# Performance work log

Hardware: AMD Instinct MI355X
Metric: run time of the kernel (lower is better)

Reference implementation:

```python
import jax, jax.numpy as jnp
import numpy as np


def setup_inputs() -> dict:
    key = jax.random.key(0)
    x = jax.random.normal(key, (4096, 16384), dtype=jnp.float32)
    return {"x": x, "k": 128}


def reference(x, k):
    # top-k along last dim, ReLU the values, scatter back into zeros
    values, indices = jax.lax.top_k(x, k)            # [N, k]
    values = jax.nn.relu(values)
    rows = jnp.arange(x.shape[0])[:, None]            # [N, 1] broadcast over k
    result = jnp.zeros_like(x).at[rows, indices].set(values)
    return result
```

## Files before the change

### kernel.cpp

```cpp
#include <hip/hip_runtime.h>

#define T 1024
#define EPT 16
#define ROWLEN 16384
#define NW (T / 64)
#define B1 4096
#define B2 1024
#define CAP 768

__device__ __forceinline__ unsigned f2ord(float f) {
    unsigned b = __float_as_uint(f);
    return b ^ ((b & 0x80000000u) ? 0xFFFFFFFFu : 0x80000000u);
}
__device__ __forceinline__ float ord2f(unsigned u) {
    unsigned b = (u & 0x80000000u) ? (u ^ 0x80000000u) : ~u;
    return __uint_as_float(b);
}

__device__ __forceinline__ void select_bin(const int* hist, int BINS, int k,
                                           int* waveSum, int* sh_b, int* sh_k) {
    const int tid  = threadIdx.x;
    const int lane = tid & 63;
    const int w    = tid >> 6;

    int bpt = (BINS + T - 1) / T;
    int lo  = tid * bpt; if (lo > BINS) lo = BINS;
    int hi  = lo + bpt;  if (hi > BINS) hi = BINS;

    int p = 0;
    for (int d = lo; d < hi; ++d) p += hist[d];

    int v = p;
    #pragma unroll
    for (int off = 1; off < 64; off <<= 1) {
        int t2 = __shfl_down(v, off);
        if (lane + off < 64) v += t2;
    }
    if (lane == 0) waveSum[w] = v;
    __syncthreads();

    int carry = 0;
    #pragma unroll
    for (int w2 = 0; w2 < NW; ++w2) if (w2 > w) carry += waveSum[w2];

    int P  = v + carry;
    int Pn = P - p;
    if (P >= k && Pn < k) {
        int running = Pn;
        for (int d = hi - 1; d >= lo; --d) {
            running += hist[d];
            if (running >= k) {
                *sh_b = d;
                *sh_k = k - (running - hist[d]);
                break;
            }
        }
    }
    __syncthreads();
}

__global__ __launch_bounds__(T, 4) void topk_relu_scatter(
        const float* __restrict__ x, const int* __restrict__ kptr,
        float* __restrict__ out) {
    __shared__ int hist[B1];
    __shared__ int waveSum[NW];
    __shared__ int sh_b, sh_k;
    __shared__ int candCnt, sh_meq, sh_cnt;
    __shared__ unsigned candU[CAP];

    const int tid = threadIdx.x;
    const int row = blockIdx.x;
    const float4* xrow = (const float4*)(x + (size_t)row * ROWLEN);
    float4*       orow = (float4*)(out + (size_t)row * ROWLEN);

    unsigned u[EPT];
    #pragma unroll
    for (int j4 = 0; j4 < EPT / 4; ++j4) {
        float4 v = xrow[tid + T * j4];
        u[4 * j4 + 0] = f2ord(v.x);
        u[4 * j4 + 1] = f2ord(v.y);
        u[4 * j4 + 2] = f2ord(v.z);
        u[4 * j4 + 3] = f2ord(v.w);
    }

    int k = *kptr;

    #pragma unroll
    for (int i = 0; i < B1 / T; ++i) hist[tid + T * i] = 0;
    if (tid == 0) candCnt = 0;
    __syncthreads();
    #pragma unroll
    for (int j = 0; j < EPT; ++j) atomicAdd(&hist[u[j] >> 20], 1);
    __syncthreads();
    select_bin(hist, B1, k, waveSum, &sh_b, &sh_k);
    const unsigned b1 = (unsigned)sh_b; k = sh_k;

    #pragma unroll
    for (int j = 0; j < EPT; ++j) {
        if ((u[j] >> 20) == b1) {
            int p = atomicAdd(&candCnt, 1);
            if (p < CAP) candU[p] = u[j];
        }
    }
    __syncthreads();
    const int m = candCnt;

    unsigned ustar; int t_eq;
    if (m <= CAP) {
        #pragma unroll
        for (int i = 0; i < B2 / T; ++i) hist[tid + T * i] = 0;
        __syncthreads();
        if (tid < m) atomicAdd(&hist[(candU[tid] >> 10) & 0x3FFu], 1);
        __syncthreads();
        select_bin(hist, B2, k, waveSum, &sh_b, &sh_k);
        const unsigned pref22 = (b1 << 10) | (unsigned)sh_b; k = sh_k;

        for (int i = 0; i < B2 / T; ++i) hist[tid + T * i] = 0;
        __syncthreads();
        if (tid < m) {
            unsigned c = candU[tid];
            if ((c >> 10) == pref22) atomicAdd(&hist[c & 0x3FFu], 1);
        }
        __syncthreads();
        select_bin(hist, B2, k, waveSum, &sh_b, &sh_k);
        ustar = (pref22 << 10) | (unsigned)sh_b;
        t_eq  = sh_k;
    } else {
        #pragma unroll
        for (int i = 0; i < B1 / T; ++i) hist[tid + T * i] = 0;
        __syncthreads();
        #pragma unroll
        for (int j = 0; j < EPT; ++j)
            if ((u[j] >> 20) == b1) atomicAdd(&hist[(u[j] >> 8) & 0xFFFu], 1);
        __syncthreads();
        select_bin(hist, B1, k, waveSum, &sh_b, &sh_k);
        const unsigned pref24 = (b1 << 12) | (unsigned)sh_b; k = sh_k;

        for (int i = tid; i < 256; i += T) hist[i] = 0;
        __syncthreads();
        #pragma unroll
        for (int j = 0; j < EPT; ++j)
            if ((u[j] >> 8) == pref24) atomicAdd(&hist[u[j] & 0xFFu], 1);
        __syncthreads();
        select_bin(hist, 256, k, waveSum, &sh_b, &sh_k);
        ustar = (pref24 << 8) | (unsigned)sh_b;
        t_eq  = sh_k;
    }

    if (tid == 0) sh_meq = 0;
    __syncthreads();
    int local = 0;
    #pragma unroll
    for (int j = 0; j < EPT; ++j) local += (u[j] == ustar);
    if (local) atomicAdd(&sh_meq, local);
    __syncthreads();
    const int meq = sh_meq;

    int idxcut;
    if (t_eq >= meq) {
        idxcut = ROWLEN;
    } else {
        int lo = 0, hi = ROWLEN - 1;
        while (lo < hi) {
            int mid = (lo + hi) >> 1;
            if (tid == 0) sh_cnt = 0;
            __syncthreads();
            int c2 = 0;
            #pragma unroll
            for (int j = 0; j < EPT; ++j) {
                int idx = 4 * (tid + T * (j >> 2)) + (j & 3);
                c2 += (u[j] == ustar && idx <= mid);
            }
            if (c2) atomicAdd(&sh_cnt, c2);
            __syncthreads();
            int cnt = sh_cnt;
            __syncthreads();
            if (cnt >= t_eq) hi = mid; else lo = mid + 1;
        }
        idxcut = lo;
    }

    #pragma unroll
    for (int j4 = 0; j4 < EPT / 4; ++j4) {
        float4 o;
        float* op = &o.x;
        #pragma unroll
        for (int c = 0; c < 4; ++c) {
            unsigned uu = u[4 * j4 + c];
            int idx = 4 * (tid + T * j4) + c;
            bool sel = (uu > ustar) || (uu == ustar && idx <= idxcut);
            float xv = ord2f(uu);
            op[c] = (sel && xv > 0.0f) ? xv : 0.0f;
        }
        orow[tid + T * j4] = o;
    }
}

extern "C" void kernel_launch(void* const* d_in, const int* in_sizes, int n_in,
                              void* d_out, int out_size, void* d_ws, size_t ws_size,
                              hipStream_t stream) {
    const float* x    = (const float*)d_in[0];
    const int*   kptr = (const int*)d_in[1];
    float*       out  = (float*)d_out;
    int rows = in_sizes[0] / ROWLEN;
    topk_relu_scatter<<<rows, T, 0, stream>>>(x, kptr, out);
}
```

Before: 477.6 us.

## Rework top-k: positive-only histogram, streaming reload, candidate rank-sort with indices

Shrinks the block to 256 threads and stops holding the row in registers, re-reading it from global memory (mostly cache hits) in each pass. The first histogram counts only positive values. Output is written in one streaming pass with nontemporal stores, and boundary-bin candidates are collected together with their indices. The cut is then resolved by an O(m^2) shared-memory rank count that scatters only the selected candidates, replacing the two extra radix passes and the tie binary search. This removes register pressure and extra synchronisation phases in exchange for more global reloads and a quadratic candidate step.

```diff
diff --git a/kernel.cpp b/kernel.cpp
--- a/kernel.cpp
+++ b/kernel.cpp
@@ -1,12 +1,13 @@
 #include <hip/hip_runtime.h>
 
-#define T 1024
-#define EPT 16
+#define T 256
+#define NW (T / 64)
 #define ROWLEN 16384
-#define NW (T / 64)
+#define EPT4 (ROWLEN / T / 4)
 #define B1 4096
-#define B2 1024
-#define CAP 768
+#define CAP 1024
+
+typedef float __attribute__((ext_vector_type(4))) f32x4;
 
 __device__ __forceinline__ unsigned f2ord(float f) {
     unsigned b = __float_as_uint(f);
@@ -59,140 +60,168 @@
     __syncthreads();
 }
 
-__global__ __launch_bounds__(T, 4) void topk_relu_scatter(
+__global__ __launch_bounds__(T, 8) void topk_relu_scatter(
         const float* __restrict__ x, const int* __restrict__ kptr,
         float* __restrict__ out) {
     __shared__ int hist[B1];
     __shared__ int waveSum[NW];
-    __shared__ int sh_b, sh_k;
-    __shared__ int candCnt, sh_meq, sh_cnt;
-    __shared__ unsigned candU[CAP];
+    __shared__ int sh_b, sh_k, candCnt, sh_npos, sh_tmp;
+    unsigned* candU = (unsigned*)&hist[2048];
+    int*      candI = &hist[3072];
 
     const int tid = threadIdx.x;
     const int row = blockIdx.x;
     const float4* xrow = (const float4*)(x + (size_t)row * ROWLEN);
     float4*       orow = (float4*)(out + (size_t)row * ROWLEN);
 
-    unsigned u[EPT];
-    #pragma unroll
-    for (int j4 = 0; j4 < EPT / 4; ++j4) {
+    const int k = *kptr;
+
+    #pragma unroll
+    for (int i = 0; i < B1 / T; ++i) hist[tid + T * i] = 0;
+    if (tid == 0) { candCnt = 0; sh_npos = 0; }
+    __syncthreads();
+
+    int npos = 0;
+    #pragma unroll
+    for (int j4 = 0; j4 < EPT4; ++j4) {
         float4 v = xrow[tid + T * j4];
-        u[4 * j4 + 0] = f2ord(v.x);
-        u[4 * j4 + 1] = f2ord(v.y);
-        u[4 * j4 + 2] = f2ord(v.z);
-        u[4 * j4 + 3] = f2ord(v.w);
-    }
-
-    int k = *kptr;
-
-    #pragma unroll
-    for (int i = 0; i < B1 / T; ++i) hist[tid + T * i] = 0;
-    if (tid == 0) candCnt = 0;
-    __syncthreads();
-    #pragma unroll
-    for (int j = 0; j < EPT; ++j) atomicAdd(&hist[u[j] >> 20], 1);
-    __syncthreads();
-    select_bin(hist, B1, k, waveSum, &sh_b, &sh_k);
-    const unsigned b1 = (unsigned)sh_b; k = sh_k;
-
-    #pragma unroll
-    for (int j = 0; j < EPT; ++j) {
-        if ((u[j] >> 20) == b1) {
-            int p = atomicAdd(&candCnt, 1);
-            if (p < CAP) candU[p] = u[j];
-        }
-    }
-    __syncthreads();
-    const int m = candCnt;
-
-    unsigned ustar; int t_eq;
-    if (m <= CAP) {
         #pragma unroll
-        for (int i = 0; i < B2 / T; ++i) hist[tid + T * i] = 0;
-        __syncthreads();
-        if (tid < m) atomicAdd(&hist[(candU[tid] >> 10) & 0x3FFu], 1);
-        __syncthreads();
-        select_bin(hist, B2, k, waveSum, &sh_b, &sh_k);
-        const unsigned pref22 = (b1 << 10) | (unsigned)sh_b; k = sh_k;
-
-        for (int i = 0; i < B2 / T; ++i) hist[tid + T * i] = 0;
-        __syncthreads();
-        if (tid < m) {
-            unsigned c = candU[tid];
-            if ((c >> 10) == pref22) atomicAdd(&hist[c & 0x3FFu], 1);
-        }
-        __syncthreads();
-        select_bin(hist, B2, k, waveSum, &sh_b, &sh_k);
-        ustar = (pref22 << 10) | (unsigned)sh_b;
-        t_eq  = sh_k;
+        for (int c = 0; c < 4; ++c) {
+            unsigned u = f2ord((&v.x)[c]);
+            if (u & 0x80000000u) {
+                ++npos;
+                atomicAdd(&hist[u >> 20], 1);
+            }
+        }
+    }
+    #pragma unroll
+    for (int off = 32; off >= 1; off >>= 1) npos += __shfl_down(npos, off);
+    if ((tid & 63) == 0) atomicAdd(&sh_npos, npos);
+    __syncthreads();
+
+    if (sh_npos >= k) {
+        select_bin(hist, B1, k, waveSum, &sh_b, &sh_k);
     } else {
         #pragma unroll
         for (int i = 0; i < B1 / T; ++i) hist[tid + T * i] = 0;
         __syncthreads();
-        #pragma unroll
-        for (int j = 0; j < EPT; ++j)
-            if ((u[j] >> 20) == b1) atomicAdd(&hist[(u[j] >> 8) & 0xFFFu], 1);
+        for (int j4 = 0; j4 < EPT4; ++j4) {
+            float4 v = xrow[tid + T * j4];
+            for (int c = 0; c < 4; ++c)
+                atomicAdd(&hist[f2ord((&v.x)[c]) >> 20], 1);
+        }
         __syncthreads();
         select_bin(hist, B1, k, waveSum, &sh_b, &sh_k);
-        const unsigned pref24 = (b1 << 12) | (unsigned)sh_b; k = sh_k;
-
-        for (int i = tid; i < 256; i += T) hist[i] = 0;
-        __syncthreads();
-        #pragma unroll
-        for (int j = 0; j < EPT; ++j)
-            if ((u[j] >> 8) == pref24) atomicAdd(&hist[u[j] & 0xFFu], 1);
-        __syncthreads();
-        select_bin(hist, 256, k, waveSum, &sh_b, &sh_k);
-        ustar = (pref24 << 8) | (unsigned)sh_b;
-        t_eq  = sh_k;
-    }
-
-    if (tid == 0) sh_meq = 0;
-    __syncthreads();
-    int local = 0;
-    #pragma unroll
-    for (int j = 0; j < EPT; ++j) local += (u[j] == ustar);
-    if (local) atomicAdd(&sh_meq, local);
-    __syncthreads();
-    const int meq = sh_meq;
-
-    int idxcut;
-    if (t_eq >= meq) {
-        idxcut = ROWLEN;
-    } else {
-        int lo = 0, hi = ROWLEN - 1;
-        while (lo < hi) {
-            int mid = (lo + hi) >> 1;
-            if (tid == 0) sh_cnt = 0;
-            __syncthreads();
-            int c2 = 0;
-            #pragma unroll
-            for (int j = 0; j < EPT; ++j) {
-                int idx = 4 * (tid + T * (j >> 2)) + (j & 3);
-                c2 += (u[j] == ustar && idx <= mid);
-            }
-            if (c2) atomicAdd(&sh_cnt, c2);
-            __syncthreads();
-            int cnt = sh_cnt;
-            __syncthreads();
-            if (cnt >= t_eq) hi = mid; else lo = mid + 1;
-        }
-        idxcut = lo;
-    }
-
-    #pragma unroll
-    for (int j4 = 0; j4 < EPT / 4; ++j4) {
+    }
+    const unsigned b1 = (unsigned)sh_b;
+    const int      kk = sh_k;
+
+    #pragma unroll
+    for (int j4 = 0; j4 < EPT4; ++j4) {
+        float4 v = xrow[tid + T * j4];
         float4 o;
-        float* op = &o.x;
         #pragma unroll
         for (int c = 0; c < 4; ++c) {
-            unsigned uu = u[4 * j4 + c];
-            int idx = 4 * (tid + T * j4) + c;
-            bool sel = (uu > ustar) || (uu == ustar && idx <= idxcut);
-            float xv = ord2f(uu);
-            op[c] = (sel && xv > 0.0f) ? xv : 0.0f;
-        }
-        orow[tid + T * j4] = o;
+            float f = (&v.x)[c];
+            unsigned u = f2ord(f);
+            unsigned bin = u >> 20;
+            (&o.x)[c] = (bin > b1 && f > 0.0f) ? f : 0.0f;
+            if (bin == b1) {
+                int p = atomicAdd(&candCnt, 1);
+                if (p < CAP) { candU[p] = u; candI[p] = 4 * (tid + T * j4) + c; }
+            }
+        }
+        __builtin_nontemporal_store(*(const f32x4*)&o, (f32x4*)&orow[tid + T * j4]);
+    }
+    __syncthreads();
+    const int m = candCnt;
+
+    if (m <= CAP) {
+        for (int i = tid; i < m; i += T) {
+            unsigned ui = candU[i]; int xi = candI[i];
+            int rank = 0;
+            for (int j = 0; j < m; ++j) {
+                unsigned uj = candU[j];
+                rank += (uj > ui) || (uj == ui && candI[j] < xi);
+            }
+            if (rank < kk) {
+                float f = ord2f(ui);
+                if (f > 0.0f) out[(size_t)row * ROWLEN + xi] = f;
+            }
+        }
+    } else {
+        unsigned pref = b1; int plen = 12; int kk2 = kk;
+        while (plen < 32) {
+            int bits = (32 - plen >= 8) ? 8 : (32 - plen);
+            int nb = 1 << bits;
+            for (int i = tid; i < nb; i += T) hist[i] = 0;
+            __syncthreads();
+            for (int j4 = 0; j4 < EPT4; ++j4) {
+                float4 v = xrow[tid + T * j4];
+                for (int c = 0; c < 4; ++c) {
+                    unsigned u = f2ord((&v.x)[c]);
+                    if ((u >> (32 - plen)) == pref)
+                        atomicAdd(&hist[(u >> (32 - plen - bits)) & (nb - 1)], 1);
+                }
+            }
+            __syncthreads();
+            select_bin(hist, nb, kk2, waveSum, &sh_b, &sh_k);
+            pref = (pref << bits) | (unsigned)sh_b;
+            kk2 = sh_k;
+            plen += bits;
+        }
+        const unsigned ustar = pref;
+        const int t_eq = kk2;
+
+        if (tid == 0) sh_tmp = 0;
+        __syncthreads();
+        {
+            int c2 = 0;
+            for (int j4 = 0; j4 < EPT4; ++j4) {
+                float4 v = xrow[tid + T * j4];
+                for (int c = 0; c < 4; ++c) c2 += (f2ord((&v.x)[c]) == ustar);
+            }
+            if (c2) atomicAdd(&sh_tmp, c2);
+        }
+        __syncthreads();
+        const int meq = sh_tmp;
+
+        int idxcut;
+        if (t_eq >= meq) {
+            idxcut = ROWLEN;
+        } else {
+            int lo = 0, hi = ROWLEN - 1;
+            while (lo < hi) {
+                int mid = (lo + hi) >> 1;
+                __syncthreads();
+                if (tid == 0) sh_tmp = 0;
+                __syncthreads();
+                int c2 = 0;
+                for (int j4 = 0; j4 < EPT4; ++j4) {
+                    float4 v = xrow[tid + T * j4];
+                    for (int c = 0; c < 4; ++c) {
+                        int idx = 4 * (tid + T * j4) + c;
+                        c2 += (f2ord((&v.x)[c]) == ustar && idx <= mid);
+                    }
+                }
+                if (c2) atomicAdd(&sh_tmp, c2);
+                __syncthreads();
+                if (sh_tmp >= t_eq) hi = mid; else lo = mid + 1;
+            }
+            idxcut = lo;
+        }
+
+        for (int j4 = 0; j4 < EPT4; ++j4) {
+            float4 v = xrow[tid + T * j4];
+            for (int c = 0; c < 4; ++c) {
+                float f = (&v.x)[c];
+                unsigned u = f2ord(f);
+                int idx = 4 * (tid + T * j4) + c;
+                bool sel = ((u >> 20) == b1 && u > ustar) ||
+                           (u == ustar && idx <= idxcut);
+                if (sel && f > 0.0f) out[(size_t)row * ROWLEN + idx] = f;
+            }
+        }
     }
 }
 
```

Result: slower. 496.8 us (+4.0%).
